# Kernel optimization log

Measured on AMD Instinct MI355X. Metric: run time of the kernel, lower is better.

## Reference

```python
import jax, jax.numpy as jnp
import numpy as np

H_DIM = 1024
N_HEADS = 16
B, T = 2, 2048
NEG = -1e9


def setup_inputs() -> dict:
    key = jax.random.key(0)
    ks = jax.random.split(key, 5)
    s = 1.0 / np.sqrt(H_DIM)
    return {
        "x": jax.random.normal(ks[0], (B, T, H_DIM), dtype=jnp.float32),
        "W_qkv": jax.random.normal(ks[1], (H_DIM, 3 * H_DIM), dtype=jnp.float32) * s,
        "b_qkv": jnp.zeros((3 * H_DIM,), dtype=jnp.float32),
        "W_proj": jax.random.normal(ks[2], (H_DIM, H_DIM), dtype=jnp.float32) * s,
        "b_proj": jnp.zeros((H_DIM,), dtype=jnp.float32),
    }


def reference(x, W_qkv, b_qkv, W_proj, b_proj):
    Bsz, Tlen, C = x.shape
    N = N_HEADS
    D = C // N
    qkv = x @ W_qkv + b_qkv                      # [B,T,3C]
    q, k, v = jnp.split(qkv, 3, axis=-1)
    # [B,T,C] -> [B,N,T,D]
    def to_heads(t):
        return t.reshape(Bsz, Tlen, N, D).transpose(0, 2, 1, 3)
    q, k, v = to_heads(q), to_heads(k), to_heads(v)
    scores = jnp.einsum('bntd,bnsd->bnts', q, k) / jnp.sqrt(jnp.float32(D))
    # additive mask exactly as original: (1 - tril) * -1e9
    mask = jnp.tril(jnp.ones((Tlen, Tlen), dtype=scores.dtype))
    scores = scores + (1.0 - mask) * NEG
    probs = jax.nn.softmax(scores, axis=-1)
    attn = jnp.einsum('bnts,bnsd->bntd', probs, v)   # [B,N,T,D]
    attn = attn.transpose(0, 2, 1, 3).reshape(Bsz, Tlen, C)
    return attn @ W_proj + b_proj
```

## Files before the change

### kernel.cpp

```cpp
#include <hip/hip_runtime.h>
#include <hip/hip_bf16.h>
#include <stdint.h>

typedef __attribute__((ext_vector_type(8))) short short8;
typedef __attribute__((ext_vector_type(4))) short s16x4;
typedef __attribute__((ext_vector_type(4))) float floatx4;
typedef __attribute__((ext_vector_type(4))) unsigned short ushortx4;

#define T_LEN 2048
#define C_DIM 1024
#define NH 16
#define HD 64

static __device__ __forceinline__ unsigned short f2bf(float f) {
  union { float f; unsigned u; } v; v.f = f;
  unsigned r = v.u + 0x7fffu + ((v.u >> 16) & 1u);
  return (unsigned short)(r >> 16);
}

static __device__ __forceinline__ void stage16(const void* g, void* l) {
  __builtin_amdgcn_global_load_lds(
      (const __attribute__((address_space(1))) void*)g,
      (__attribute__((address_space(3))) void*)l, 16, 0, 0);
}

static __device__ __forceinline__ floatx4 mfma16(s16x4 a, s16x4 b, floatx4 c) {
  asm("v_mfma_f32_16x16x16_bf16 %0, %1, %2, %0" : "+v"(c) : "v"(a), "v"(b));
  return c;
}
static __device__ __forceinline__ unsigned cvt_pk_bf16(float lo, float hi) {
  unsigned r;
  asm("v_cvt_pk_bf16_f32 %0, %1, %2" : "=v"(r) : "v"(lo), "v"(hi));
  return r;
}

static __device__ __forceinline__ void tc_body(
    const float* __restrict__ in, unsigned short* __restrict__ out,
    int R, int C, int bx, int by, int tid, unsigned short (*tile)[72]) {
  const int r0 = by * 64;
  const int c0 = bx * 64;
#pragma unroll
  for (int e = 0; e < 4; ++e) {
    const int ch = e * 256 + tid;
    const int r = ch >> 4, c4 = (ch & 15) * 4;
    const float4 v = *(const float4*)(in + (long)(r0 + r) * C + c0 + c4);
    tile[r][c4 + 0] = f2bf(v.x);
    tile[r][c4 + 1] = f2bf(v.y);
    tile[r][c4 + 2] = f2bf(v.z);
    tile[r][c4 + 3] = f2bf(v.w);
  }
  __syncthreads();
#pragma unroll
  for (int e = 0; e < 2; ++e) {
    const int ch = e * 256 + tid;
    const int c = ch >> 3, k8 = (ch & 7) * 8;
    short8 w;
#pragma unroll
    for (int j = 0; j < 8; ++j) w[j] = (short)tile[k8 + j][c];
    *(short8*)(out + (long)(c0 + c) * R + r0 + k8) = w;
  }
}

__global__ __launch_bounds__(256) void prep(
    const float* __restrict__ x, unsigned short* __restrict__ xbf,
    const float* __restrict__ Wqkv, unsigned short* __restrict__ Wqkvt,
    const float* __restrict__ Wproj, unsigned short* __restrict__ Wprojt) {
  __shared__ unsigned short tile[64][72];
  const int bid = (int)blockIdx.x;
  const int tid = (int)threadIdx.x;
  if (bid < 4096) {
    const long i = ((long)bid * 256 + tid) * 4;
    const float4 v = *(const float4*)(x + i);
    ushortx4 o;
    o[0] = f2bf(v.x); o[1] = f2bf(v.y); o[2] = f2bf(v.z); o[3] = f2bf(v.w);
    *(ushortx4*)(xbf + i) = o;
  } else if (bid < 4096 + 768) {
    const int t = bid - 4096;
    tc_body(Wqkv, Wqkvt, 1024, 3072, t % 48, t / 48, tid, tile);
  } else {
    const int t = bid - 4864;
    tc_body(Wproj, Wprojt, 1024, 1024, t % 16, t / 16, tid, tile);
  }
}

#define GSTAGE(BUF, K0) do {                                                          \
    _Pragma("unroll") for (int r = 0; r < 2; ++r) {                                   \
      const int ch = r * 256 + tid;                                                   \
      const int trow = ch >> 2, tcol = (ch & 3) * 8;                                  \
      stage16(Abase + (long)trow * K + (K0) + tcol, &As[BUF][(r * 256 + wid * 64) * 8]); \
      stage16(Bbase + (long)trow * K + (K0) + tcol, &Bs[BUF][(r * 256 + wid * 64) * 8]); \
    } } while (0)

template <int MODE>
__global__ __launch_bounds__(256) void gemm_bt(
    const unsigned short* __restrict__ A,
    const unsigned short* __restrict__ Bt,
    const float* __restrict__ bias,
    int M, int N, int K, int nbx,
    unsigned short* __restrict__ q_out,
    unsigned short* __restrict__ k_out,
    unsigned short* __restrict__ v_out,
    float* __restrict__ f_out) {
  __shared__ unsigned short As[2][128 * 32];
  __shared__ unsigned short Bs[2][128 * 32];
  const int tid = threadIdx.x;
  const int lane = tid & 63;
  const int wid = tid >> 6;
  const int wr = wid >> 1, wc = wid & 1;
  const int lrow = lane & 15, lgrp = lane >> 4;
  const int bid = (int)blockIdx.x;
  const int v = (bid & 7) * ((int)gridDim.x >> 3) + (bid >> 3);
  const long row0 = (long)(v / nbx) * 128;
  const long col0 = (long)(v % nbx) * 128;

  floatx4 acc[4][4];
#pragma unroll
  for (int m = 0; m < 4; ++m)
#pragma unroll
    for (int n = 0; n < 4; ++n)
      acc[m][n] = (floatx4){0.f, 0.f, 0.f, 0.f};

  const unsigned short* Abase = A + row0 * K;
  const unsigned short* Bbase = Bt + col0 * K;
  const int NT = K >> 5;

  GSTAGE(0, 0);
  asm volatile("s_waitcnt vmcnt(0)" ::: "memory");
  __builtin_amdgcn_s_barrier();

  int cur = 0;
  for (int t = 0; t < NT - 1; ++t) {
    GSTAGE(cur ^ 1, (t + 1) * 32);
    short8 af[4], bf[4];
#pragma unroll
    for (int m = 0; m < 4; ++m)
      af[m] = *(const short8*)&As[cur][(wr * 64 + m * 16 + lrow) * 32 + lgrp * 8];
#pragma unroll
    for (int n = 0; n < 4; ++n)
      bf[n] = *(const short8*)&Bs[cur][(wc * 64 + n * 16 + lrow) * 32 + lgrp * 8];
    __builtin_amdgcn_s_setprio(1);
#pragma unroll
    for (int m = 0; m < 4; ++m)
#pragma unroll
      for (int n = 0; n < 4; ++n)
        acc[m][n] = __builtin_amdgcn_mfma_f32_16x16x32_bf16(af[m], bf[n], acc[m][n], 0, 0, 0);
    __builtin_amdgcn_s_setprio(0);
    asm volatile("s_waitcnt vmcnt(0)" ::: "memory");
    __builtin_amdgcn_s_barrier();
    cur ^= 1;
  }
  {
    short8 af[4], bf[4];
#pragma unroll
    for (int m = 0; m < 4; ++m)
      af[m] = *(const short8*)&As[cur][(wr * 64 + m * 16 + lrow) * 32 + lgrp * 8];
#pragma unroll
    for (int n = 0; n < 4; ++n)
      bf[n] = *(const short8*)&Bs[cur][(wc * 64 + n * 16 + lrow) * 32 + lgrp * 8];
#pragma unroll
    for (int m = 0; m < 4; ++m)
#pragma unroll
      for (int n = 0; n < 4; ++n)
        acc[m][n] = __builtin_amdgcn_mfma_f32_16x16x32_bf16(af[m], bf[n], acc[m][n], 0, 0, 0);
  }

  if (MODE == 0) {
#pragma unroll
    for (int n = 0; n < 4; ++n) {
      const int c = (int)col0 + wc * 64 + n * 16 + lrow;
      const float bs = bias[c];
      const int sect = c >> 10;
      const int h = (c & 1023) >> 6;
      const int d = c & 63;
      const float scl = sect == 0 ? 0.18033688011112042f : 1.0f;
#pragma unroll
      for (int m = 0; m < 4; ++m) {
        if (sect == 2) {
          const long r0m = row0 + wr * 64 + m * 16 + lgrp * 4;
          const long b = r0m >> 11;
          const long t0 = r0m & 2047;
          ushortx4 pk;
#pragma unroll
          for (int i = 0; i < 4; ++i) pk[i] = f2bf(acc[m][n][i] + bs);
          *(ushortx4*)&v_out[((b * NH + h) * HD + d) * T_LEN + t0] = pk;
        } else {
          unsigned short* dst = sect == 0 ? q_out : k_out;
#pragma unroll
          for (int i = 0; i < 4; ++i) {
            const long r = row0 + wr * 64 + m * 16 + lgrp * 4 + i;
            const long b = r >> 11;
            const long t = r & 2047;
            dst[((b * NH + h) * T_LEN + t) * HD + d] = f2bf((acc[m][n][i] + bs) * scl);
          }
        }
      }
    }
  } else {
#pragma unroll
    for (int n = 0; n < 4; ++n) {
      const int c = (int)col0 + wc * 64 + n * 16 + lrow;
      const float bs = bias[c];
#pragma unroll
      for (int m = 0; m < 4; ++m) {
#pragma unroll
        for (int i = 0; i < 4; ++i) {
          const long r = row0 + wr * 64 + m * 16 + lgrp * 4 + i;
          f_out[r * (long)N + c] = acc[m][n][i] + bs;
        }
      }
    }
  }
}

__global__ __launch_bounds__(256) void attn_fwd(
    const unsigned short* __restrict__ Qb,
    const unsigned short* __restrict__ Kb,
    const unsigned short* __restrict__ Vt,
    unsigned short* __restrict__ attn) {
  __shared__ unsigned short Ks[2][4096];
  __shared__ unsigned short Vs[2][4096];
  const int bid = (int)blockIdx.x;
  const int xcd = bid & 7;
  const int j = bid >> 3;
  const int bh = xcd * 4 + (j & 3);
  const int qblk = 15 - (j >> 2);
  const int b = bh >> 4, h = bh & 15;
  const int tid = (int)threadIdx.x;
  const int wid = tid >> 6;
  const int lane = tid & 63;
  const int lrow = lane & 15, lgrp = lane >> 4;
  const int q0 = qblk * 128 + wid * 32;
  const int myext = q0 + 32;
  const int blksteps = (qblk * 128 + 128) >> 6;

  const unsigned short* Qh = Qb + (long)bh * T_LEN * HD;
  const unsigned short* Kh = Kb + (long)bh * T_LEN * HD;
  const unsigned short* Vh = Vt + (long)bh * HD * T_LEN;

  int koff[2], voff[2];
#pragma unroll
  for (int jj = 0; jj < 2; ++jj) {
    const int c = wid * 128 + jj * 64 + lane;
    const int row = c >> 3;
    const int cs = ((c & 7) ^ (row & 7)) * 8;
    koff[jj] = row * HD + cs;
    voff[jj] = row * T_LEN + cs;
  }

#define ASTAGE(BUF, S0) do {                                                         \
    _Pragma("unroll") for (int jj = 0; jj < 2; ++jj)                                 \
      stage16(Kh + (long)(S0) * HD + koff[jj], &Ks[BUF][(wid * 128 + jj * 64) * 8]); \
    _Pragma("unroll") for (int jj = 0; jj < 2; ++jj)                                 \
      stage16(Vh + (long)(S0) + voff[jj], &Vs[BUF][(wid * 128 + jj * 64) * 8]);      \
  } while (0)

  short8 aq[2][2];
#pragma unroll
  for (int qs = 0; qs < 2; ++qs)
#pragma unroll
    for (int kk = 0; kk < 2; ++kk)
      aq[qs][kk] = *(const short8*)(Qh + (long)(q0 + qs * 16 + lrow) * HD + kk * 32 + lgrp * 8);

  float m_i[2] = {-1e30f, -1e30f};
  float s_i[2] = {0.f, 0.f};
  floatx4 o[2][4];
#pragma unroll
  for (int qs = 0; qs < 2; ++qs)
#pragma unroll
    for (int d0 = 0; d0 < 4; ++d0) o[qs][d0] = (floatx4){0.f, 0.f, 0.f, 0.f};

  ASTAGE(0, 0);
  asm volatile("s_waitcnt vmcnt(0)" ::: "memory");
  __builtin_amdgcn_s_barrier();

  int cur = 0;
  for (int st = 0; st < blksteps; ++st) {
    const int s0 = st * 64;
    if (st + 1 < blksteps) ASTAGE(cur ^ 1, s0 + 64);
    if (s0 < myext) {
      floatx4 sf[2][4];
#pragma unroll
      for (int qs = 0; qs < 2; ++qs)
#pragma unroll
        for (int sc = 0; sc < 4; ++sc) sf[qs][sc] = (floatx4){0.f, 0.f, 0.f, 0.f};
      __builtin_amdgcn_s_setprio(1);
#pragma unroll
      for (int sc = 0; sc < 4; ++sc) {
        const int row = sc * 16 + lrow;
        const int rsw = row & 7;
        const short8 k0 = *(const short8*)&Ks[cur][row * 64 + (lgrp ^ rsw) * 8];
        const short8 k1 = *(const short8*)&Ks[cur][row * 64 + ((4 + lgrp) ^ rsw) * 8];
        sf[0][sc] = __builtin_amdgcn_mfma_f32_16x16x32_bf16(k0, aq[0][0], sf[0][sc], 0, 0, 0);
        sf[1][sc] = __builtin_amdgcn_mfma_f32_16x16x32_bf16(k0, aq[1][0], sf[1][sc], 0, 0, 0);
        sf[0][sc] = __builtin_amdgcn_mfma_f32_16x16x32_bf16(k1, aq[0][1], sf[0][sc], 0, 0, 0);
        sf[1][sc] = __builtin_amdgcn_mfma_f32_16x16x32_bf16(k1, aq[1][1], sf[1][sc], 0, 0, 0);
      }
      __builtin_amdgcn_s_setprio(0);
      if (s0 + 64 > q0) {
#pragma unroll
        for (int qs = 0; qs < 2; ++qs) {
          const int q = q0 + qs * 16 + lrow;
#pragma unroll
          for (int sc = 0; sc < 4; ++sc) {
#pragma unroll
            for (int i = 0; i < 4; ++i) {
              const int s = s0 + sc * 16 + lgrp * 4 + i;
              if (s > q) sf[qs][sc][i] = -1e30f;
            }
          }
        }
      }
      s16x4 pa[2][4];
#pragma unroll
      for (int qs = 0; qs < 2; ++qs) {
        float m0 = fmaxf(fmaxf(sf[qs][0][0], sf[qs][0][1]), fmaxf(sf[qs][0][2], sf[qs][0][3]));
        float m1 = fmaxf(fmaxf(sf[qs][1][0], sf[qs][1][1]), fmaxf(sf[qs][1][2], sf[qs][1][3]));
        float m2 = fmaxf(fmaxf(sf[qs][2][0], sf[qs][2][1]), fmaxf(sf[qs][2][2], sf[qs][2][3]));
        float m3 = fmaxf(fmaxf(sf[qs][3][0], sf[qs][3][1]), fmaxf(sf[qs][3][2], sf[qs][3][3]));
        float mm = fmaxf(fmaxf(m0, m1), fmaxf(m2, m3));
        mm = fmaxf(mm, __shfl_xor(mm, 16));
        mm = fmaxf(mm, __shfl_xor(mm, 32));
        const int grow = !__all(mm <= m_i[qs]);
        float scale = 1.0f;
        if (grow) {
          const float mnew = fmaxf(m_i[qs], mm);
          scale = exp2f(m_i[qs] - mnew);
          m_i[qs] = mnew;
        }
        float rs = 0.f;
#pragma unroll
        for (int sc = 0; sc < 4; ++sc) {
#pragma unroll
          for (int i = 0; i < 4; ++i) {
            const float pv = exp2f(sf[qs][sc][i] - m_i[qs]);
            sf[qs][sc][i] = pv;
            rs += pv;
          }
        }
        rs += __shfl_xor(rs, 16);
        rs += __shfl_xor(rs, 32);
        s_i[qs] = s_i[qs] * scale + rs;
        if (grow) {
#pragma unroll
          for (int i = 0; i < 4; ++i) {
            const float sbc = __shfl(scale, 4 * lgrp + i);
#pragma unroll
            for (int d0 = 0; d0 < 4; ++d0) o[qs][d0][i] *= sbc;
          }
        }
#pragma unroll
        for (int sc = 0; sc < 4; ++sc) {
          union { unsigned u[2]; s16x4 v; } tmp;
          tmp.u[0] = cvt_pk_bf16(sf[qs][sc][0], sf[qs][sc][1]);
          tmp.u[1] = cvt_pk_bf16(sf[qs][sc][2], sf[qs][sc][3]);
          pa[qs][sc] = tmp.v;
        }
      }
      __builtin_amdgcn_s_setprio(1);
#pragma unroll
      for (int d0 = 0; d0 < 4; ++d0) {
        const int d = d0 * 16 + lrow;
        const int dsw = d & 7;
#pragma unroll
        for (int sc = 0; sc < 4; ++sc) {
          const int g = sc * 2 + (lgrp >> 1);
          const s16x4 vb = *(const s16x4*)&Vs[cur][d * 64 + ((g ^ dsw)) * 8 + (lgrp & 1) * 4];
          o[0][d0] = mfma16(pa[0][sc], vb, o[0][d0]);
          o[1][d0] = mfma16(pa[1][sc], vb, o[1][d0]);
        }
      }
      __builtin_amdgcn_s_setprio(0);
    }
    asm volatile("s_waitcnt vmcnt(0)" ::: "memory");
    __builtin_amdgcn_s_barrier();
    cur ^= 1;
  }
#undef ASTAGE

#pragma unroll
  for (int qs = 0; qs < 2; ++qs) {
    float inv[4];
#pragma unroll
    for (int i = 0; i < 4; ++i) inv[i] = 1.0f / __shfl(s_i[qs], 4 * lgrp + i);
#pragma unroll
    for (int d0 = 0; d0 < 4; ++d0) {
#pragma unroll
      for (int i = 0; i < 4; ++i) {
        const int q = q0 + qs * 16 + lgrp * 4 + i;
        attn[(long)(b * T_LEN + q) * C_DIM + h * HD + d0 * 16 + lrow] =
            f2bf(o[qs][d0][i] * inv[i]);
      }
    }
  }
}

extern "C" void kernel_launch(void* const* d_in, const int* in_sizes, int n_in,
                              void* d_out, int out_size, void* d_ws, size_t ws_size,
                              hipStream_t stream) {
  const float* x     = (const float*)d_in[0];
  const float* Wqkv  = (const float*)d_in[1];
  const float* bqkv  = (const float*)d_in[2];
  const float* Wproj = (const float*)d_in[3];
  const float* bproj = (const float*)d_in[4];
  float* out = (float*)d_out;
  char* ws = (char*)d_ws;
  const size_t MB = 1024 * 1024;
  unsigned short* Qb     = (unsigned short*)(ws + 0 * MB);
  unsigned short* Kb     = (unsigned short*)(ws + 8 * MB);
  unsigned short* Vt     = (unsigned short*)(ws + 24 * MB);
  unsigned short* attn   = (unsigned short*)(ws + 32 * MB);
  unsigned short* xbf    = (unsigned short*)(ws + 40 * MB);
  unsigned short* Wqkvt  = (unsigned short*)(ws + 48 * MB);
  unsigned short* Wprojt = (unsigned short*)(ws + 54 * MB);

  prep<<<5120, 256, 0, stream>>>(x, xbf, Wqkv, Wqkvt, Wproj, Wprojt);
  gemm_bt<0><<<768, 256, 0, stream>>>(xbf, Wqkvt, bqkv, 4096, 3072, 1024, 24,
                                      Qb, Kb, Vt, nullptr);
  attn_fwd<<<512, 256, 0, stream>>>(Qb, Kb, Vt, attn);
  gemm_bt<1><<<256, 256, 0, stream>>>(attn, Wprojt, bproj, 4096, 1024, 1024, 8,
                                      nullptr, nullptr, nullptr, out);
}
```

Before: 217.0 us.

## Halve attention query tile to 64 rows and double grid size

The attention kernel now gives each block 64 query rows (16 per wave) instead of 128 (32 per wave), and launches 1024 blocks instead of 512. The goal is more parallelism and finer causal load balance across the 256 CUs, with fewer registers per wave. The cost is that each staged K/V tile is reused by half as many queries, so LDS staging traffic and global K/V reads per FLOP roughly double.

```diff
diff --git a/kernel.cpp b/kernel.cpp
--- a/kernel.cpp
+++ b/kernel.cpp
@@ -223,15 +223,15 @@
   const int xcd = bid & 7;
   const int j = bid >> 3;
   const int bh = xcd * 4 + (j & 3);
-  const int qblk = 15 - (j >> 2);
+  const int qblk = 31 - (j >> 2);
   const int b = bh >> 4, h = bh & 15;
   const int tid = (int)threadIdx.x;
   const int wid = tid >> 6;
   const int lane = tid & 63;
   const int lrow = lane & 15, lgrp = lane >> 4;
-  const int q0 = qblk * 128 + wid * 32;
-  const int myext = q0 + 32;
-  const int blksteps = (qblk * 128 + 128) >> 6;
+  const int q0 = qblk * 64 + wid * 16;
+  const int myext = q0 + 16;
+  const int blksteps = qblk + 1;
 
   const unsigned short* Qh = Qb + (long)bh * T_LEN * HD;
   const unsigned short* Kh = Kb + (long)bh * T_LEN * HD;
@@ -254,20 +254,16 @@
       stage16(Vh + (long)(S0) + voff[jj], &Vs[BUF][(wid * 128 + jj * 64) * 8]);      \
   } while (0)
 
-  short8 aq[2][2];
-#pragma unroll
-  for (int qs = 0; qs < 2; ++qs)
-#pragma unroll
-    for (int kk = 0; kk < 2; ++kk)
-      aq[qs][kk] = *(const short8*)(Qh + (long)(q0 + qs * 16 + lrow) * HD + kk * 32 + lgrp * 8);
-
-  float m_i[2] = {-1e30f, -1e30f};
-  float s_i[2] = {0.f, 0.f};
-  floatx4 o[2][4];
-#pragma unroll
-  for (int qs = 0; qs < 2; ++qs)
-#pragma unroll
-    for (int d0 = 0; d0 < 4; ++d0) o[qs][d0] = (floatx4){0.f, 0.f, 0.f, 0.f};
+  short8 aq[2];
+#pragma unroll
+  for (int kk = 0; kk < 2; ++kk)
+    aq[kk] = *(const short8*)(Qh + (long)(q0 + lrow) * HD + kk * 32 + lgrp * 8);
+
+  float m_i = -1e30f;
+  float s_i = 0.f;
+  floatx4 o[4];
+#pragma unroll
+  for (int d0 = 0; d0 < 4; ++d0) o[d0] = (floatx4){0.f, 0.f, 0.f, 0.f};
 
   ASTAGE(0, 0);
   asm volatile("s_waitcnt vmcnt(0)" ::: "memory");
@@ -278,11 +274,9 @@
     const int s0 = st * 64;
     if (st + 1 < blksteps) ASTAGE(cur ^ 1, s0 + 64);
     if (s0 < myext) {
-      floatx4 sf[2][4];
-#pragma unroll
-      for (int qs = 0; qs < 2; ++qs)
-#pragma unroll
-        for (int sc = 0; sc < 4; ++sc) sf[qs][sc] = (floatx4){0.f, 0.f, 0.f, 0.f};
+      floatx4 sf[4];
+#pragma unroll
+      for (int sc = 0; sc < 4; ++sc) sf[sc] = (floatx4){0.f, 0.f, 0.f, 0.f};
       __builtin_amdgcn_s_setprio(1);
 #pragma unroll
       for (int sc = 0; sc < 4; ++sc) {
@@ -290,71 +284,63 @@
         const int rsw = row & 7;
         const short8 k0 = *(const short8*)&Ks[cur][row * 64 + (lgrp ^ rsw) * 8];
         const short8 k1 = *(const short8*)&Ks[cur][row * 64 + ((4 + lgrp) ^ rsw) * 8];
-        sf[0][sc] = __builtin_amdgcn_mfma_f32_16x16x32_bf16(k0, aq[0][0], sf[0][sc], 0, 0, 0);
-        sf[1][sc] = __builtin_amdgcn_mfma_f32_16x16x32_bf16(k0, aq[1][0], sf[1][sc], 0, 0, 0);
-        sf[0][sc] = __builtin_amdgcn_mfma_f32_16x16x32_bf16(k1, aq[0][1], sf[0][sc], 0, 0, 0);
-        sf[1][sc] = __builtin_amdgcn_mfma_f32_16x16x32_bf16(k1, aq[1][1], sf[1][sc], 0, 0, 0);
+        sf[sc] = __builtin_amdgcn_mfma_f32_16x16x32_bf16(k0, aq[0], sf[sc], 0, 0, 0);
+        sf[sc] = __builtin_amdgcn_mfma_f32_16x16x32_bf16(k1, aq[1], sf[sc], 0, 0, 0);
       }
       __builtin_amdgcn_s_setprio(0);
       if (s0 + 64 > q0) {
-#pragma unroll
-        for (int qs = 0; qs < 2; ++qs) {
-          const int q = q0 + qs * 16 + lrow;
-#pragma unroll
-          for (int sc = 0; sc < 4; ++sc) {
-#pragma unroll
-            for (int i = 0; i < 4; ++i) {
-              const int s = s0 + sc * 16 + lgrp * 4 + i;
-              if (s > q) sf[qs][sc][i] = -1e30f;
-            }
+        const int q = q0 + lrow;
+#pragma unroll
+        for (int sc = 0; sc < 4; ++sc) {
+#pragma unroll
+          for (int i = 0; i < 4; ++i) {
+            const int s = s0 + sc * 16 + lgrp * 4 + i;
+            if (s > q) sf[sc][i] = -1e30f;
           }
         }
       }
-      s16x4 pa[2][4];
-#pragma unroll
-      for (int qs = 0; qs < 2; ++qs) {
-        float m0 = fmaxf(fmaxf(sf[qs][0][0], sf[qs][0][1]), fmaxf(sf[qs][0][2], sf[qs][0][3]));
-        float m1 = fmaxf(fmaxf(sf[qs][1][0], sf[qs][1][1]), fmaxf(sf[qs][1][2], sf[qs][1][3]));
-        float m2 = fmaxf(fmaxf(sf[qs][2][0], sf[qs][2][1]), fmaxf(sf[qs][2][2], sf[qs][2][3]));
-        float m3 = fmaxf(fmaxf(sf[qs][3][0], sf[qs][3][1]), fmaxf(sf[qs][3][2], sf[qs][3][3]));
-        float mm = fmaxf(fmaxf(m0, m1), fmaxf(m2, m3));
-        mm = fmaxf(mm, __shfl_xor(mm, 16));
-        mm = fmaxf(mm, __shfl_xor(mm, 32));
-        const int grow = !__all(mm <= m_i[qs]);
-        float scale = 1.0f;
-        if (grow) {
-          const float mnew = fmaxf(m_i[qs], mm);
-          scale = exp2f(m_i[qs] - mnew);
-          m_i[qs] = mnew;
-        }
-        float rs = 0.f;
-#pragma unroll
-        for (int sc = 0; sc < 4; ++sc) {
-#pragma unroll
-          for (int i = 0; i < 4; ++i) {
-            const float pv = exp2f(sf[qs][sc][i] - m_i[qs]);
-            sf[qs][sc][i] = pv;
-            rs += pv;
-          }
-        }
-        rs += __shfl_xor(rs, 16);
-        rs += __shfl_xor(rs, 32);
-        s_i[qs] = s_i[qs] * scale + rs;
-        if (grow) {
-#pragma unroll
-          for (int i = 0; i < 4; ++i) {
-            const float sbc = __shfl(scale, 4 * lgrp + i);
-#pragma unroll
-            for (int d0 = 0; d0 < 4; ++d0) o[qs][d0][i] *= sbc;
-          }
-        }
-#pragma unroll
-        for (int sc = 0; sc < 4; ++sc) {
-          union { unsigned u[2]; s16x4 v; } tmp;
-          tmp.u[0] = cvt_pk_bf16(sf[qs][sc][0], sf[qs][sc][1]);
-          tmp.u[1] = cvt_pk_bf16(sf[qs][sc][2], sf[qs][sc][3]);
-          pa[qs][sc] = tmp.v;
-        }
+      float m0 = fmaxf(fmaxf(sf[0][0], sf[0][1]), fmaxf(sf[0][2], sf[0][3]));
+      float m1 = fmaxf(fmaxf(sf[1][0], sf[1][1]), fmaxf(sf[1][2], sf[1][3]));
+      float m2 = fmaxf(fmaxf(sf[2][0], sf[2][1]), fmaxf(sf[2][2], sf[2][3]));
+      float m3 = fmaxf(fmaxf(sf[3][0], sf[3][1]), fmaxf(sf[3][2], sf[3][3]));
+      float mm = fmaxf(fmaxf(m0, m1), fmaxf(m2, m3));
+      mm = fmaxf(mm, __shfl_xor(mm, 16));
+      mm = fmaxf(mm, __shfl_xor(mm, 32));
+      const int grow = !__all(mm <= m_i);
+      float scale = 1.0f;
+      if (grow) {
+        const float mnew = fmaxf(m_i, mm);
+        scale = exp2f(m_i - mnew);
+        m_i = mnew;
+      }
+      float rs = 0.f;
+      s16x4 pa[4];
+#pragma unroll
+      for (int sc = 0; sc < 4; ++sc) {
+#pragma unroll
+        for (int i = 0; i < 4; ++i) {
+          const float pv = exp2f(sf[sc][i] - m_i);
+          sf[sc][i] = pv;
+          rs += pv;
+        }
+      }
+      rs += __shfl_xor(rs, 16);
+      rs += __shfl_xor(rs, 32);
+      s_i = s_i * scale + rs;
+      if (grow) {
+#pragma unroll
+        for (int i = 0; i < 4; ++i) {
+          const float sbc = __shfl(scale, 4 * lgrp + i);
+#pragma unroll
+          for (int d0 = 0; d0 < 4; ++d0) o[d0][i] *= sbc;
+        }
+      }
+#pragma unroll
+      for (int sc = 0; sc < 4; ++sc) {
+        union { unsigned u[2]; s16x4 v; } tmp;
+        tmp.u[0] = cvt_pk_bf16(sf[sc][0], sf[sc][1]);
+        tmp.u[1] = cvt_pk_bf16(sf[sc][2], sf[sc][3]);
+        pa[sc] = tmp.v;
       }
       __builtin_amdgcn_s_setprio(1);
 #pragma unroll
@@ -365,8 +351,7 @@
         for (int sc = 0; sc < 4; ++sc) {
           const int g = sc * 2 + (lgrp >> 1);
           const s16x4 vb = *(const s16x4*)&Vs[cur][d * 64 + ((g ^ dsw)) * 8 + (lgrp & 1) * 4];
-          o[0][d0] = mfma16(pa[0][sc], vb, o[0][d0]);
-          o[1][d0] = mfma16(pa[1][sc], vb, o[1][d0]);
+          o[d0] = mfma16(pa[sc], vb, o[d0]);
         }
       }
       __builtin_amdgcn_s_setprio(0);
@@ -377,19 +362,16 @@
   }
 #undef ASTAGE
 
-#pragma unroll
-  for (int qs = 0; qs < 2; ++qs) {
-    float inv[4];
-#pragma unroll
-    for (int i = 0; i < 4; ++i) inv[i] = 1.0f / __shfl(s_i[qs], 4 * lgrp + i);
-#pragma unroll
-    for (int d0 = 0; d0 < 4; ++d0) {
-#pragma unroll
-      for (int i = 0; i < 4; ++i) {
-        const int q = q0 + qs * 16 + lgrp * 4 + i;
-        attn[(long)(b * T_LEN + q) * C_DIM + h * HD + d0 * 16 + lrow] =
-            f2bf(o[qs][d0][i] * inv[i]);
-      }
+  float inv[4];
+#pragma unroll
+  for (int i = 0; i < 4; ++i) inv[i] = 1.0f / __shfl(s_i, 4 * lgrp + i);
+#pragma unroll
+  for (int d0 = 0; d0 < 4; ++d0) {
+#pragma unroll
+    for (int i = 0; i < 4; ++i) {
+      const int q = q0 + lgrp * 4 + i;
+      attn[(long)(b * T_LEN + q) * C_DIM + h * HD + d0 * 16 + lrow] =
+          f2bf(o[d0][i] * inv[i]);
     }
   }
 }
@@ -416,7 +398,7 @@
   prep<<<5120, 256, 0, stream>>>(x, xbf, Wqkv, Wqkvt, Wproj, Wprojt);
   gemm_bt<0><<<768, 256, 0, stream>>>(xbf, Wqkvt, bqkv, 4096, 3072, 1024, 24,
                                       Qb, Kb, Vt, nullptr);
-  attn_fwd<<<512, 256, 0, stream>>>(Qb, Kb, Vt, attn);
+  attn_fwd<<<1024, 256, 0, stream>>>(Qb, Kb, Vt, attn);
   gemm_bt<1><<<256, 256, 0, stream>>>(attn, Wprojt, bproj, 4096, 1024, 1024, 8,
                                       nullptr, nullptr, nullptr, out);
 }
```

New measurement: 197.4 us. -9.0%, faster.
